# Kernel tuning notes

Measured on AMD Instinct MI355X. Metric: run time of the kernel, lower is better.

## Reference

```python
import jax, jax.numpy as jnp
import numpy as np

PI = 3.141592653589793
N = 4194304


def _lerp(a, b, w):
    return a + w * (b - a)


def _schlick(u):
    m = jnp.clip(1.0 - u, 0.0, 1.0)
    return m ** 5


def setup_inputs() -> dict:
    key = jax.random.key(0)
    kl, kv, kp = jax.random.split(key, 3)

    def unit_dirs(k):
        v = jax.random.normal(k, (N, 3), dtype=jnp.float32)
        v = v / jnp.linalg.norm(v, axis=-1, keepdims=True)
        # upper hemisphere so most samples pass the cos_nl/cos_nv >= 0 test
        return v.at[:, 2].set(jnp.abs(v[:, 2]))

    light = unit_dirs(kl)
    view = unit_dirs(kv)
    inputs = jnp.stack([light, view], axis=1)  # [N, 2, 3]

    return {
        "inputs": inputs,
        "base_color": jnp.array([0.8, 0.8, 0.8], dtype=jnp.float32),
        "metallic": jnp.array([0.3], dtype=jnp.float32),
        "subsurface": jnp.array([0.2], dtype=jnp.float32),
        "specular": jnp.array([0.5], dtype=jnp.float32),
        "roughness": jnp.array([0.5], dtype=jnp.float32),
        "specular_tint": jnp.array([0.1], dtype=jnp.float32),
        "anisotropic": jnp.array([0.2], dtype=jnp.float32),
        "sheen": jnp.array([0.3], dtype=jnp.float32),
        "sheen_tint": jnp.array([0.5], dtype=jnp.float32),
        "clear_coat": jnp.array([0.5], dtype=jnp.float32),
        "clear_coat_gloss": jnp.array([0.8], dtype=jnp.float32),
    }


def _brdf(inputs, base_color, metallic, subsurface, specular, roughness,
          specular_tint, anisotropic, sheen, sheen_tint, clear_coat,
          clear_coat_gloss):
    # scalar params
    mtl = metallic[0]; sub = subsurface[0]; spec = specular[0]
    rough = roughness[0]; sp_tint = specular_tint[0]; aniso = anisotropic[0]
    sh = sheen[0]; sh_tint = sheen_tint[0]; cc = clear_coat[0]
    cc_gloss = clear_coat_gloss[0]

    light = inputs[:, 0, :]  # [N, 3]
    view = inputs[:, 1, :]   # [N, 3]
    hv = light + view
    half = hv / jnp.linalg.norm(hv, axis=-1, keepdims=True)

    # tangent x=[1,0,0], bitangent y=[0,1,0], normal=[0,0,1]
    cos_nl = light[:, 2]
    cos_nv = view[:, 2]
    cos_nh = half[:, 2]
    cos_hl = jnp.sum(half * light, axis=-1)

    valid = (cos_nl >= 0) & (cos_nv >= 0)
    # grad-safe cosines for invalid (masked-out) samples
    cnl = jnp.where(valid, cos_nl, 0.5)
    cnv = jnp.where(valid, cos_nv, 0.5)

    cd_lin = base_color ** 2.2  # mon2lin
    cd_lum = 0.3 * cd_lin[0] + 0.6 * cd_lin[1] + 0.1 * cd_lin[2]
    c_tint = jnp.where(cd_lum > 0, cd_lin / jnp.maximum(cd_lum, 1e-20),
                       jnp.zeros(3, cd_lin.dtype))

    c_spec0 = _lerp(spec * 0.08 * _lerp(1.0, c_tint, sp_tint), cd_lin, mtl)  # [3]
    c_sheen = _lerp(1.0, c_tint, sh_tint)  # [3]

    fl = _schlick(cnl)
    fv = _schlick(cnv)
    fd90 = 0.5 + 2.0 * cos_hl ** 2 * rough
    fd = _lerp(1.0, fd90, fl) * _lerp(1.0, fd90, fv)
    fss90 = cos_hl ** 2 * rough
    fss = _lerp(1.0, fss90, fl) * _lerp(1.0, fss90, fv)
    ss = 1.25 * (fss * (1.0 / (cnl + cnv) - 0.5) + 0.5)

    aspect = jnp.sqrt(1.0 - aniso * 0.9)
    ax = jnp.maximum(0.001, rough ** 2 / aspect)
    ay = jnp.maximum(0.001, rough ** 2 * aspect)

    # GTR2 anisotropic distribution
    Ds = 1.0 / (PI * ax * ay * ((half[:, 0] / ax) ** 2 +
                                (half[:, 1] / ay) ** 2 + cos_nh ** 2) ** 2)
    FH = _schlick(cos_hl)
    Fs = _lerp(c_spec0[None, :], 1.0, FH[:, None])  # [N, 3]

    def g_aniso(c, cx, cy):
        return 1.0 / (c + jnp.sqrt((cx * ax) ** 2 + (cy * ay) ** 2 + c ** 2))

    Gs = g_aniso(cnl, light[:, 0], light[:, 1]) * g_aniso(cnv, view[:, 0], view[:, 1])
    specular_term = (Gs * Ds)[:, None] * Fs

    Fsheen = FH[:, None] * sh * c_sheen[None, :]
    diffuse = ((1.0 / PI) * _lerp(fd, ss, sub)[:, None] * cd_lin[None, :] +
               Fsheen) * (1.0 - mtl)

    # clearcoat: GTR1 with a = lerp(0.1, 0.001, gloss)
    a_cc = _lerp(0.1, 0.001, cc_gloss)
    a2 = a_cc ** 2
    t = 1.0 + (a2 - 1.0) * cos_nh ** 2
    Dr = jnp.where(a_cc >= 1.0, 1.0 / PI, (a2 - 1.0) / (PI * jnp.log(a2) * t))

    def g025(c):
        a = 0.0625  # 0.25^2
        return 1.0 / (c + jnp.sqrt(a + c ** 2 - a * c ** 2))

    Gr = g025(cnl) * g025(cnv)
    Fr = _lerp(0.04, 1.0, FH)
    clear = 0.25 * cc * Gr * Fr * Dr

    out = diffuse + specular_term + clear[:, None]
    return jnp.where(valid[:, None], out, 0.0)


@jax.jit
def reference(inputs, base_color, metallic, subsurface, specular, roughness,
              specular_tint, anisotropic, sheen, sheen_tint, clear_coat,
              clear_coat_gloss):
    return _brdf(inputs, base_color, metallic, subsurface, specular, roughness,
                 specular_tint, anisotropic, sheen, sheen_tint, clear_coat,
                 clear_coat_gloss)
```

## Files before the change

kernel.cpp:

```cpp
#include <hip/hip_runtime.h>

#define PI_F 3.14159265358979323846f

__device__ __forceinline__ float rcpf_(float x){ return __builtin_amdgcn_rcpf(x); }
__device__ __forceinline__ float sqrtf_(float x){ return __builtin_amdgcn_sqrtf(x); }

__device__ __forceinline__ float schlick5(float u){
    float m = 1.0f - u;
    float m2 = m * m;
    return m2 * m2 * m;
}

__device__ __forceinline__ void compute_uniforms(
    const float* bc, float mtl, float sub, float spec, float rough,
    float sp_tint, float aniso, float sh, float sh_tint, float cc, float ccg,
    float* u)
{
    const float cd0 = __powf(bc[0], 2.2f);
    const float cd1 = __powf(bc[1], 2.2f);
    const float cd2 = __powf(bc[2], 2.2f);
    const float lum = 0.3f*cd0 + 0.6f*cd1 + 0.1f*cd2;
    const float il  = rcpf_(fmaxf(lum, 1e-20f));
    const float ct0 = (lum > 0.f) ? cd0*il : 0.f;
    const float ct1 = (lum > 0.f) ? cd1*il : 0.f;
    const float ct2 = (lum > 0.f) ? cd2*il : 0.f;

    const float s008 = spec * 0.08f;
    const float b0 = s008 * (1.f + sp_tint*(ct0 - 1.f));
    const float b1 = s008 * (1.f + sp_tint*(ct1 - 1.f));
    const float b2 = s008 * (1.f + sp_tint*(ct2 - 1.f));
    const float cs0_0 = b0 + mtl*(cd0 - b0);
    const float cs0_1 = b1 + mtl*(cd1 - b1);
    const float cs0_2 = b2 + mtl*(cd2 - b2);

    const float om = 1.f - mtl;
    const float invpi = 1.f / PI_F;

    const float aspect = sqrtf_(1.f - aniso*0.9f);
    const float r2 = rough * rough;
    const float ax = fmaxf(0.001f, r2 * rcpf_(aspect));
    const float ay = fmaxf(0.001f, r2 * aspect);

    const float a_cc = 0.1f + (0.001f - 0.1f)*ccg;
    const float a2 = a_cc * a_cc;
    float a2m1, k_dr;
    if (a_cc >= 1.0f) { a2m1 = 0.f; k_dr = invpi; }
    else              { a2m1 = a2 - 1.f; k_dr = (a2 - 1.f) * rcpf_(PI_F * __logf(a2)); }

    u[0] = rough;
    u[1] = sub;
    u[2] = ax*ax;
    u[3] = ay*ay;
    u[4] = rcpf_(ax*ax);
    u[5] = rcpf_(ay*ay);
    u[6] = rcpf_(PI_F * ax * ay);
    u[7] = a2m1;
    u[8] = k_dr;
    u[9] = 0.25f * cc;
    u[10] = cd0 * om * invpi;
    u[11] = cd1 * om * invpi;
    u[12] = cd2 * om * invpi;
    u[13] = sh * (1.f + sh_tint*(ct0 - 1.f)) * om;
    u[14] = sh * (1.f + sh_tint*(ct1 - 1.f)) * om;
    u[15] = sh * (1.f + sh_tint*(ct2 - 1.f)) * om;
    u[16] = cs0_0;
    u[17] = cs0_1;
    u[18] = cs0_2;
    u[19] = 1.f - cs0_0;
    u[20] = 1.f - cs0_1;
    u[21] = 1.f - cs0_2;
}

__global__ void setup_kernel(
    const float* __restrict__ bc, const float* __restrict__ metallic,
    const float* __restrict__ subsurface, const float* __restrict__ specular,
    const float* __restrict__ roughness, const float* __restrict__ specular_tint,
    const float* __restrict__ anisotropic, const float* __restrict__ sheen,
    const float* __restrict__ sheen_tint, const float* __restrict__ clear_coat,
    const float* __restrict__ clear_coat_gloss, float* __restrict__ ws)
{
    if (threadIdx.x == 0) {
        float u[22];
        compute_uniforms(bc, metallic[0], subsurface[0], specular[0], roughness[0],
                         specular_tint[0], anisotropic[0], sheen[0], sheen_tint[0],
                         clear_coat[0], clear_coat_gloss[0], u);
        #pragma unroll
        for (int i = 0; i < 22; ++i) ws[i] = u[i];
    }
}

__global__ __launch_bounds__(256, 4) void brdf_kernel(
    const float* __restrict__ in,
    const float* __restrict__ uws,
    float* __restrict__ out,
    int npts)
{
    float U[22];
    #pragma unroll
    for (int i = 0; i < 22; ++i) U[i] = uws[i];

    const float rough   = U[0],  sub     = U[1];
    const float ax2     = U[2],  ay2     = U[3];
    const float inv_ax2 = U[4],  inv_ay2 = U[5];
    const float k_ds    = U[6],  a2m1    = U[7];
    const float k_dr    = U[8],  cc_q    = U[9];
    const float two_rough = 2.f * rough;

    int t = blockIdx.x * blockDim.x + threadIdx.x;
    if ((long)t * 4 >= npts) return;

    const float4* in4 = reinterpret_cast<const float4*>(in) + (size_t)t * 6;
    float4 q0 = in4[0], q1 = in4[1], q2 = in4[2], q3 = in4[3], q4 = in4[4], q5 = in4[5];

    auto shade = [&](float l0, float l1, float l2, float v0, float v1, float v2,
                     float& o0, float& o1, float& o2) {
        const float hvx = l0 + v0, hvy = l1 + v1, hvz = l2 + v2;
        const float n2 = hvx*hvx + hvy*hvy + hvz*hvz;
        const float chl = 0.5f * sqrtf_(n2);
        const float chl2 = 0.25f * n2;

        const bool valid = (l2 >= 0.f) && (v2 >= 0.f);
        const float cnl = valid ? l2 : 0.5f;
        const float cnv = valid ? v2 : 0.5f;

        const float fl = schlick5(cnl);
        const float fv = schlick5(cnv);
        const float FH = schlick5(chl);

        const float fd90m1  = two_rough * chl2 - 0.5f;
        const float fd  = (1.f + fd90m1*fl) * (1.f + fd90m1*fv);
        const float fss90m1 = rough * chl2 - 1.f;
        const float fss = (1.f + fss90m1*fl) * (1.f + fss90m1*fv);
        const float ss = 1.25f * (fss * (rcpf_(cnl + cnv) - 0.5f) + 0.5f);
        const float dw = fd + sub * (ss - fd);

        const float dtermu = hvx*hvx*inv_ax2 + hvy*hvy*inv_ay2 + hvz*hvz;
        const float denL = cnl + sqrtf_(l0*l0*ax2 + l1*l1*ay2 + cnl*cnl);
        const float denV = cnv + sqrtf_(v0*v0*ax2 + v1*v1*ay2 + cnv*cnv);
        const float GsDs = k_ds * (n2 * n2) * rcpf_(dtermu*dtermu * denL * denV);

        const float tden = n2 + a2m1 * (hvz*hvz);
        const float grL = cnl + sqrtf_(0.0625f + 0.9375f*cnl*cnl);
        const float grV = cnv + sqrtf_(0.0625f + 0.9375f*cnv*cnv);
        const float Fr = 0.04f + 0.96f * FH;
        const float clear = cc_q * Fr * k_dr * n2 * rcpf_(tden * grL * grV);

        float r0 = dw*U[10] + FH*U[13] + GsDs*(U[16] + FH*U[19]) + clear;
        float r1 = dw*U[11] + FH*U[14] + GsDs*(U[17] + FH*U[20]) + clear;
        float r2 = dw*U[12] + FH*U[15] + GsDs*(U[18] + FH*U[21]) + clear;

        o0 = valid ? r0 : 0.f;
        o1 = valid ? r1 : 0.f;
        o2 = valid ? r2 : 0.f;
    };

    float a0,a1,a2v, b0,b1,b2v, c0,c1,c2v, d0,d1,d2v;
    shade(q0.x,q0.y,q0.z, q0.w,q1.x,q1.y, a0,a1,a2v);
    shade(q1.z,q1.w,q2.x, q2.y,q2.z,q2.w, b0,b1,b2v);
    shade(q3.x,q3.y,q3.z, q3.w,q4.x,q4.y, c0,c1,c2v);
    shade(q4.z,q4.w,q5.x, q5.y,q5.z,q5.w, d0,d1,d2v);

    float4* out4 = reinterpret_cast<float4*>(out) + (size_t)t * 3;
    out4[0] = make_float4(a0, a1, a2v, b0);
    out4[1] = make_float4(b1, b2v, c0, c1);
    out4[2] = make_float4(c2v, d0, d1, d2v);
}

extern "C" void kernel_launch(void* const* d_in, const int* in_sizes, int n_in,
                              void* d_out, int out_size, void* d_ws, size_t ws_size,
                              hipStream_t stream) {
    const float* in = (const float*)d_in[0];
    const int npts = in_sizes[0] / 6;
    const int nthreads = npts / 4;
    const int block = 256;
    const int grid = (nthreads + block - 1) / block;

    float* ws = (float*)d_ws;
    setup_kernel<<<1, 64, 0, stream>>>(
        (const float*)d_in[1], (const float*)d_in[2], (const float*)d_in[3],
        (const float*)d_in[4], (const float*)d_in[5], (const float*)d_in[6],
        (const float*)d_in[7], (const float*)d_in[8], (const float*)d_in[9],
        (const float*)d_in[10], (const float*)d_in[11], ws);

    brdf_kernel<<<grid, block, 0, stream>>>(in, ws, (float*)d_out, npts);
}
```

Before: 188.4 us.

## Stage input and output through shared memory for coalesced global access

Each block loads its tile of light/view vectors into LDS with contiguous float4 loads, shades two points per thread from LDS, then writes results back through LDS with contiguous float2 stores. This targets the uncoalesced 96-byte-strided per-thread global loads and stores of the previous layout. In exchange it adds two block barriers, LDS traffic with strided (bank-conflicting) accesses, and halves per-thread work.

```diff
diff --git a/kernel.cpp b/kernel.cpp
--- a/kernel.cpp
+++ b/kernel.cpp
@@ -1,6 +1,8 @@
 #include <hip/hip_runtime.h>
 
 #define PI_F 3.14159265358979323846f
+#define THREADS 256
+#define PTS_PER_BLOCK 512
 
 __device__ __forceinline__ float rcpf_(float x){ return __builtin_amdgcn_rcpf(x); }
 __device__ __forceinline__ float sqrtf_(float x){ return __builtin_amdgcn_sqrtf(x); }
@@ -89,16 +91,20 @@
     }
 }
 
-__global__ __launch_bounds__(256, 4) void brdf_kernel(
+__global__ __launch_bounds__(THREADS, 4) void brdf_kernel(
     const float* __restrict__ in,
     const float* __restrict__ uws,
     float* __restrict__ out,
     int npts)
 {
+    __shared__ float4 s_in4[PTS_PER_BLOCK * 6 / 4];
+    __shared__ float2 s_out2[PTS_PER_BLOCK * 3 / 2];
+    float* s_in = reinterpret_cast<float*>(s_in4);
+    float* s_out = reinterpret_cast<float*>(s_out2);
+
     float U[22];
     #pragma unroll
     for (int i = 0; i < 22; ++i) U[i] = uws[i];
-
     const float rough   = U[0],  sub     = U[1];
     const float ax2     = U[2],  ay2     = U[3];
     const float inv_ax2 = U[4],  inv_ay2 = U[5];
@@ -106,14 +112,25 @@
     const float k_dr    = U[8],  cc_q    = U[9];
     const float two_rough = 2.f * rough;
 
-    int t = blockIdx.x * blockDim.x + threadIdx.x;
-    if ((long)t * 4 >= npts) return;
-
-    const float4* in4 = reinterpret_cast<const float4*>(in) + (size_t)t * 6;
-    float4 q0 = in4[0], q1 = in4[1], q2 = in4[2], q3 = in4[3], q4 = in4[4], q5 = in4[5];
-
-    auto shade = [&](float l0, float l1, float l2, float v0, float v1, float v2,
-                     float& o0, float& o1, float& o2) {
+    const int j = threadIdx.x;
+    const size_t blk = blockIdx.x;
+
+    const size_t total_f4 = (size_t)npts * 6 / 4;
+    const float4* gin = reinterpret_cast<const float4*>(in);
+    const size_t f4_base = blk * (PTS_PER_BLOCK * 6 / 4);
+    #pragma unroll
+    for (int k = 0; k < 3; ++k) {
+        size_t idx = f4_base + j + k * THREADS;
+        if (idx < total_f4) s_in4[j + k * THREADS] = gin[idx];
+    }
+    __syncthreads();
+
+    #pragma unroll
+    for (int k = 0; k < 2; ++k) {
+        const int p = j + k * THREADS;
+        const float l0 = s_in[6*p+0], l1 = s_in[6*p+1], l2 = s_in[6*p+2];
+        const float v0 = s_in[6*p+3], v1 = s_in[6*p+4], v2 = s_in[6*p+5];
+
         const float hvx = l0 + v0, hvy = l1 + v1, hvz = l2 + v2;
         const float n2 = hvx*hvx + hvy*hvy + hvz*hvz;
         const float chl = 0.5f * sqrtf_(n2);
@@ -149,21 +166,20 @@
         float r1 = dw*U[11] + FH*U[14] + GsDs*(U[17] + FH*U[20]) + clear;
         float r2 = dw*U[12] + FH*U[15] + GsDs*(U[18] + FH*U[21]) + clear;
 
-        o0 = valid ? r0 : 0.f;
-        o1 = valid ? r1 : 0.f;
-        o2 = valid ? r2 : 0.f;
-    };
-
-    float a0,a1,a2v, b0,b1,b2v, c0,c1,c2v, d0,d1,d2v;
-    shade(q0.x,q0.y,q0.z, q0.w,q1.x,q1.y, a0,a1,a2v);
-    shade(q1.z,q1.w,q2.x, q2.y,q2.z,q2.w, b0,b1,b2v);
-    shade(q3.x,q3.y,q3.z, q3.w,q4.x,q4.y, c0,c1,c2v);
-    shade(q4.z,q4.w,q5.x, q5.y,q5.z,q5.w, d0,d1,d2v);
-
-    float4* out4 = reinterpret_cast<float4*>(out) + (size_t)t * 3;
-    out4[0] = make_float4(a0, a1, a2v, b0);
-    out4[1] = make_float4(b1, b2v, c0, c1);
-    out4[2] = make_float4(c2v, d0, d1, d2v);
+        s_out[3*p+0] = valid ? r0 : 0.f;
+        s_out[3*p+1] = valid ? r1 : 0.f;
+        s_out[3*p+2] = valid ? r2 : 0.f;
+    }
+    __syncthreads();
+
+    const size_t total_f2 = (size_t)npts * 3 / 2;
+    float2* gout = reinterpret_cast<float2*>(out);
+    const size_t f2_base = blk * (PTS_PER_BLOCK * 3 / 2);
+    #pragma unroll
+    for (int k = 0; k < 3; ++k) {
+        size_t idx = f2_base + j + k * THREADS;
+        if (idx < total_f2) gout[idx] = s_out2[j + k * THREADS];
+    }
 }
 
 extern "C" void kernel_launch(void* const* d_in, const int* in_sizes, int n_in,
@@ -171,9 +187,7 @@
                               hipStream_t stream) {
     const float* in = (const float*)d_in[0];
     const int npts = in_sizes[0] / 6;
-    const int nthreads = npts / 4;
-    const int block = 256;
-    const int grid = (nthreads + block - 1) / block;
+    const int grid = (npts + PTS_PER_BLOCK - 1) / PTS_PER_BLOCK;
 
     float* ws = (float*)d_ws;
     setup_kernel<<<1, 64, 0, stream>>>(
@@ -182,5 +196,5 @@
         (const float*)d_in[7], (const float*)d_in[8], (const float*)d_in[9],
         (const float*)d_in[10], (const float*)d_in[11], ws);
 
-    brdf_kernel<<<grid, block, 0, stream>>>(in, ws, (float*)d_out, npts);
-}
+    brdf_kernel<<<grid, THREADS, 0, stream>>>(in, ws, (float*)d_out, npts);
+}
```

After: 181.7 us. -3.5%, faster.
